# Kernel optimization log

Measured on AMD Instinct MI355X. Metric: run time of the kernel, lower is better.

The kernel has to match this reference:

```python
import jax, jax.numpy as jnp
import numpy as np

QMAX = 127.0
EPS = 1e-12


def _smooth_quant(x, col_scale):
    """Per-row int8 quantization of (x * col_scale).
    Returns (q, row_scale): q holds integer values in [-127, 127] (kept in f32,
    exactly representable), row_scale is abs-max/127 per row."""
    xs = x * col_scale                                  # [R, K]
    row_scale = jnp.max(jnp.abs(xs), axis=-1) / QMAX    # [R]
    row_scale = jnp.maximum(row_scale, EPS)
    q = jnp.clip(jnp.round(xs / row_scale[:, None]), -QMAX, QMAX)
    return q, row_scale


def setup_inputs() -> dict:
    key = jax.random.key(0)
    k1, k2, k3 = jax.random.split(key, 3)
    B, S, K, N = 4, 8192, 1024, 1024
    input_ = jax.random.normal(k1, (B, S, K), dtype=jnp.float32)
    weight = jax.random.normal(k2, (N, K), dtype=jnp.float32) * 0.02
    bias = jax.random.normal(k3, (N,), dtype=jnp.float32) * 0.01
    return {"input": input_, "weight": weight, "bias": bias}


def reference(input, weight, bias):
    x2 = input.reshape(-1, input.shape[-1])             # [M, K]
    # SmoothQuant smoothing scale: sqrt(colmax(|x|) * colmax(|w|)), shape [K]
    in_max = jnp.max(jnp.abs(x2), axis=0)
    w_max = jnp.max(jnp.abs(weight), axis=0)
    smooth_scale = jnp.sqrt(jnp.maximum(in_max * w_max, EPS))
    # quantize activations divided by smooth_scale, weights multiplied by it
    x_q, x_s = _smooth_quant(x2, 1.0 / smooth_scale)    # [M,K], [M]
    w_q, w_s = _smooth_quant(weight, smooth_scale)      # [N,K], [N]
    # int8 matmul (emulated exactly in f32) + row/col dequant scales + bias
    acc = x_q @ w_q.T                                   # [M, N]
    out = acc * x_s[:, None] * w_s[None, :] + bias
    return out.reshape(*input.shape[:-1], weight.shape[0])
```

## Files before the change

### kernel.cpp

```cpp
#include <hip/hip_runtime.h>


typedef int v4i __attribute__((ext_vector_type(4)));

__device__ __forceinline__ void gld_lds16(const void* g, void* l) {
    __builtin_amdgcn_global_load_lds(
        (const __attribute__((address_space(1))) void*)g,
        (__attribute__((address_space(3))) void*)l,
        16, 0, 0);
}

__device__ __forceinline__ void colmax_body(const float* __restrict__ src,
                                            int r0, int r1, int K,
                                            float* __restrict__ dst) {
    const int c = threadIdx.x * 4;
    float m0 = 0.f, m1 = 0.f, m2 = 0.f, m3 = 0.f;
    const float* p = src + (size_t)r0 * K + c;
#pragma unroll 8
    for (int r = r0; r < r1; ++r, p += K) {
        float4 v = *(const float4*)p;
        m0 = fmaxf(m0, fabsf(v.x));
        m1 = fmaxf(m1, fabsf(v.y));
        m2 = fmaxf(m2, fabsf(v.z));
        m3 = fmaxf(m3, fabsf(v.w));
    }
    float4 o; o.x = m0; o.y = m1; o.z = m2; o.w = m3;
    *(float4*)(dst + c) = o;
}

__global__ __launch_bounds__(256) void colmax_part_kernel(const float* __restrict__ src,
                                                          int rows, int rpb, int K,
                                                          float* __restrict__ partial) {
    int r0 = blockIdx.x * rpb;
    int r1 = r0 + rpb; if (r1 > rows) r1 = rows;
    colmax_body(src, r0, r1, K, partial + (size_t)blockIdx.x * K);
}

__global__ __launch_bounds__(256) void part2_fused_kernel(const float* __restrict__ p1x, int nx,
                                                          const float* __restrict__ w, int nw,
                                                          float* __restrict__ p2x,
                                                          float* __restrict__ pw, int K) {
    const int b = blockIdx.x;
    if (b < 16) {
        const int rpb = nx >> 4;
        colmax_body(p1x, b * rpb, (b + 1) * rpb, K, p2x + (size_t)b * K);
    } else {
        const int rpb = nw >> 4;
        colmax_body(w, (b - 16) * rpb, (b - 15) * rpb, K, pw + (size_t)(b - 16) * K);
    }
}

__global__ void finalize_kernel(const float* __restrict__ px, int nx,
                                const float* __restrict__ pw, int nw,
                                float* __restrict__ smooth, float* __restrict__ inv_s, int K) {
    int c = blockIdx.x * blockDim.x + threadIdx.x;
    if (c >= K) return;
    float mx = 0.f, mw = 0.f;
    for (int r = 0; r < nx; ++r) mx = fmaxf(mx, px[(size_t)r * K + c]);
    for (int r = 0; r < nw; ++r) mw = fmaxf(mw, pw[(size_t)r * K + c]);
    float s = sqrtf(fmaxf(mx * mw, 1e-12f));
    smooth[c] = s;
    inv_s[c]  = 1.0f / s;
}

__device__ __forceinline__ void quant_row_body(const float* __restrict__ src,
                                               const float* __restrict__ colscale,
                                               signed char* __restrict__ q,
                                               float* __restrict__ rowscale,
                                               int row, int K, int lane) {
    const float* srow = src + (size_t)row * K + lane * 16;
    const float* crow = colscale + lane * 16;
    float xs[16];
    float mv = 0.f;
#pragma unroll
    for (int i = 0; i < 4; ++i) {
        float4 v  = *(const float4*)(srow + i * 4);
        float4 cs = *(const float4*)(crow + i * 4);
        xs[i*4+0] = v.x * cs.x; xs[i*4+1] = v.y * cs.y;
        xs[i*4+2] = v.z * cs.z; xs[i*4+3] = v.w * cs.w;
        mv = fmaxf(mv, fmaxf(fmaxf(fabsf(xs[i*4+0]), fabsf(xs[i*4+1])),
                             fmaxf(fabsf(xs[i*4+2]), fabsf(xs[i*4+3]))));
    }
#pragma unroll
    for (int off = 32; off > 0; off >>= 1)
        mv = fmaxf(mv, __shfl_xor(mv, off, 64));
    const float rs = fmaxf(mv / 127.0f, 1e-12f);
    unsigned pk[4];
#pragma unroll
    for (int i = 0; i < 4; ++i) {
        float q0 = fminf(fmaxf(rintf(xs[i*4+0] / rs), -127.f), 127.f);
        float q1 = fminf(fmaxf(rintf(xs[i*4+1] / rs), -127.f), 127.f);
        float q2 = fminf(fmaxf(rintf(xs[i*4+2] / rs), -127.f), 127.f);
        float q3 = fminf(fmaxf(rintf(xs[i*4+3] / rs), -127.f), 127.f);
        int b0 = (int)q0, b1 = (int)q1, b2 = (int)q2, b3 = (int)q3;
        pk[i] = (unsigned)(b0 & 0xff) | ((unsigned)(b1 & 0xff) << 8)
              | ((unsigned)(b2 & 0xff) << 16) | ((unsigned)(b3 & 0xff) << 24);
    }
    *(uint4*)(q + (size_t)row * K + lane * 16) = make_uint4(pk[0], pk[1], pk[2], pk[3]);
    if (lane == 0) rowscale[row] = rs;
}

__global__ __launch_bounds__(256) void quant_fused_kernel(
    const float* __restrict__ w, const float* __restrict__ x,
    const float* __restrict__ smooth, const float* __restrict__ inv_s,
    signed char* __restrict__ w_q, float* __restrict__ w_s,
    signed char* __restrict__ x_q, float* __restrict__ x_s,
    int K, int wblocks) {
    const int wave = threadIdx.x >> 6, lane = threadIdx.x & 63;
    const int b = blockIdx.x;
    if (b < wblocks) {
        quant_row_body(w, smooth, w_q, w_s, b * 4 + wave, K, lane);
    } else {
        quant_row_body(x, inv_s, x_q, x_s, (b - wblocks) * 4 + wave, K, lane);
    }
}

__global__ __launch_bounds__(256, 2) void gemm_i8_kernel(
    const signed char* __restrict__ Aq,
    const signed char* __restrict__ Bq,
    const float* __restrict__ xs,
    const float* __restrict__ wsc,
    const float* __restrict__ bias,
    float* __restrict__ out,
    int M, int N, int K) {
    __shared__ __align__(16) signed char As[32768];
    __shared__ __align__(16) signed char Bs[32768];

    const int tid  = threadIdx.x;
    const int lane = tid & 63;
    const int wave = tid >> 6;
    const int wm = wave >> 1;
    const int wn = wave & 1;
    const int g  = lane >> 4;
    const int fr = lane & 15;

    const int NT = K >> 7;

    const int nwg = gridDim.x;
    const int wg  = (blockIdx.x & 7) * (nwg >> 3) + (blockIdx.x >> 3);
    const int nTn = N >> 7;
    const int tm = wg / nTn, tn = wg % nTn;
    const int bm = tm << 7, bn = tn << 7;

    const int srow = tid >> 2;
    const int schk = (tid & 3) ^ (srow & 3);
    const signed char* srcA0 = Aq + (size_t)(bm + srow) * K + schk * 16;
    const signed char* srcA1 = srcA0 + (size_t)64 * K;
    const signed char* srcB0 = Bq + (size_t)(bn + srow) * K + schk * 16;
    const signed char* srcB1 = srcB0 + (size_t)64 * K;
    const int ldsSt = tid * 16;

    const int swz   = (g ^ (fr & 3)) * 16;
    const int aBase = (wm * 64 + fr) * 64 + swz;
    const int bBase = (wn * 64 + fr) * 64 + swz;

    v4i acc[4][4] = {};
    v4i bf[4];

#define STAGE_A(T, KS) do { \
        const int go_ = (T) * 128 + (KS) * 64; \
        signed char* l_ = &As[((T) & 1) * 16384 + (KS) * 8192 + ldsSt]; \
        gld_lds16(srcA0 + go_, l_); \
        gld_lds16(srcA1 + go_, l_ + 4096); \
    } while (0)
#define STAGE_B(T, KS) do { \
        const int go_ = (T) * 128 + (KS) * 64; \
        signed char* l_ = &Bs[((T) & 1) * 16384 + (KS) * 8192 + ldsSt]; \
        gld_lds16(srcB0 + go_, l_); \
        gld_lds16(srcB1 + go_, l_ + 4096); \
    } while (0)

#define PHASE(BUF, KS, MH, STG, WAIT) \
    do { \
        const int hb_ = (BUF) * 16384 + (KS) * 8192; \
        v4i af[2]; \
        _Pragma("unroll") \
        for (int i = 0; i < 2; ++i) \
            af[i] = *(const v4i*)&As[hb_ + aBase + ((MH) * 2 + i) * 1024]; \
        if ((MH) == 0) { \
            _Pragma("unroll") \
            for (int j = 0; j < 4; ++j) \
                bf[j] = *(const v4i*)&Bs[hb_ + bBase + j * 1024]; \
        } \
        STG; \
        asm volatile("s_waitcnt " WAIT ::: "memory"); \
        asm volatile("s_barrier" ::: "memory"); \
        asm volatile("s_waitcnt lgkmcnt(0)" ::: "memory"); \
        __builtin_amdgcn_sched_barrier(0); \
        __builtin_amdgcn_s_setprio(1); \
        _Pragma("unroll") \
        for (int i = 0; i < 2; ++i) \
            _Pragma("unroll") \
            for (int j = 0; j < 4; ++j) \
                acc[(MH) * 2 + i][j] = __builtin_amdgcn_mfma_i32_16x16x64_i8( \
                    af[i], bf[j], acc[(MH) * 2 + i][j], 0, 0, 0); \
        __builtin_amdgcn_s_setprio(0); \
        asm volatile("s_barrier" ::: "memory"); \
    } while (0)

    STAGE_A(0, 0); STAGE_B(0, 0);
    STAGE_A(0, 1); STAGE_B(0, 1);
    STAGE_A(1, 0); STAGE_B(1, 0);
    asm volatile("s_waitcnt vmcnt(4)" ::: "memory");
    asm volatile("s_barrier" ::: "memory");

    for (int t = 0; t < NT - 2; ++t) {
        const int buf = t & 1;
        PHASE(buf, 0, 0, STAGE_A(t + 1, 1), "vmcnt(8)");
        PHASE(buf, 0, 1, STAGE_B(t + 1, 1), "vmcnt(8)");
        PHASE(buf, 1, 0, STAGE_A(t + 2, 0), "vmcnt(8)");
        PHASE(buf, 1, 1, STAGE_B(t + 2, 0), "vmcnt(8)");
    }
    {
        const int t = NT - 2, buf = t & 1;
        PHASE(buf, 0, 0, STAGE_A(t + 1, 1), "vmcnt(8)");
        PHASE(buf, 0, 1, STAGE_B(t + 1, 1), "vmcnt(8)");
        PHASE(buf, 1, 0, (void)0, "vmcnt(8)");
        PHASE(buf, 1, 1, (void)0, "vmcnt(4)");
    }
    {
        const int buf = (NT - 1) & 1;
        PHASE(buf, 0, 0, (void)0, "vmcnt(4)");
        PHASE(buf, 0, 1, (void)0, "vmcnt(0)");
        PHASE(buf, 1, 0, (void)0, "vmcnt(0)");
        PHASE(buf, 1, 1, (void)0, "vmcnt(0)");
    }
#undef PHASE
#undef STAGE_A
#undef STAGE_B

    const int orow0 = bm + wm * 64 + g * 4;
    const int ocol0 = bn + wn * 64 + fr;
    float wv[4], bvv[4];
#pragma unroll
    for (int j = 0; j < 4; ++j) {
        wv[j]  = wsc[ocol0 + j * 16];
        bvv[j] = bias[ocol0 + j * 16];
    }
#pragma unroll
    for (int i = 0; i < 4; ++i) {
#pragma unroll
        for (int r = 0; r < 4; ++r) {
            const int row = orow0 + i * 16 + r;
            const float xv = xs[row];
            float* op = out + (size_t)row * N + ocol0;
#pragma unroll
            for (int j = 0; j < 4; ++j)
                op[j * 16] = (float)acc[i][j][r] * xv * wv[j] + bvv[j];
        }
    }
}

extern "C" void kernel_launch(void* const* d_in, const int* in_sizes, int n_in,
                              void* d_out, int out_size, void* d_ws, size_t ws_size,
                              hipStream_t stream) {
    const float* x    = (const float*)d_in[0];
    const float* w    = (const float*)d_in[1];
    const float* bias = (const float*)d_in[2];
    float* out = (float*)d_out;

    const int N = in_sizes[2];
    const int K = in_sizes[1] / N;
    const int M = in_sizes[0] / K;

    char* ws = (char*)d_ws;
    float* p1x       = (float*)(ws);
    float* p2x       = (float*)(ws + 2097152);
    float* pw        = (float*)(ws + 2162688);
    float* smooth    = (float*)(ws + 2228224);
    float* inv_s     = (float*)(ws + 2232320);
    float* w_s       = (float*)(ws + 2236416);
    float* x_s       = (float*)(ws + 2240512);
    signed char* x_q = (signed char*)(ws + 2371584);
    signed char* w_q = x_q + (size_t)M * K;

    colmax_part_kernel<<<512, 256, 0, stream>>>(x, M, 64, K, p1x);
    part2_fused_kernel<<<32, 256, 0, stream>>>(p1x, 512, w, N, p2x, pw, K);
    finalize_kernel<<<(K + 255) / 256, 256, 0, stream>>>(p2x, 16, pw, 16, smooth, inv_s, K);
    quant_fused_kernel<<<N / 4 + M / 4, 256, 0, stream>>>(w, x, smooth, inv_s,
                                                          w_q, w_s, x_q, x_s, K, N / 4);
    gemm_i8_kernel<<<(M / 128) * (N / 128), 256, 0, stream>>>(x_q, w_q, x_s, w_s, bias, out, M, N, K);
}
```

Measured before the change: 321.3 us.

## Use 8-wave 512-thread GEMM workgroups with 64x32 per-wave tiles and merged staging

```diff
diff --git a/kernel.cpp b/kernel.cpp
--- a/kernel.cpp
+++ b/kernel.cpp
@@ -115,7 +115,7 @@
     }
 }
 
-__global__ __launch_bounds__(256, 2) void gemm_i8_kernel(
+__global__ __launch_bounds__(512, 4) void gemm_i8_kernel(
     const signed char* __restrict__ Aq,
     const signed char* __restrict__ Bq,
     const float* __restrict__ xs,
@@ -129,8 +129,8 @@
     const int tid  = threadIdx.x;
     const int lane = tid & 63;
     const int wave = tid >> 6;
-    const int wm = wave >> 1;
-    const int wn = wave & 1;
+    const int wm = wave >> 2;
+    const int wn = wave & 3;
     const int g  = lane >> 4;
     const int fr = lane & 15;
 
@@ -143,97 +143,94 @@
     const int bm = tm << 7, bn = tn << 7;
 
     const int srow = tid >> 2;
-    const int schk = (tid & 3) ^ (srow & 3);
+    const int schk = (tid & 3) ^ ((tid >> 3) & 3);
     const signed char* srcA0 = Aq + (size_t)(bm + srow) * K + schk * 16;
-    const signed char* srcA1 = srcA0 + (size_t)64 * K;
     const signed char* srcB0 = Bq + (size_t)(bn + srow) * K + schk * 16;
-    const signed char* srcB1 = srcB0 + (size_t)64 * K;
     const int ldsSt = tid * 16;
 
-    const int swz   = (g ^ (fr & 3)) * 16;
+    const int swz   = (g ^ ((fr >> 1) & 3)) * 16;
     const int aBase = (wm * 64 + fr) * 64 + swz;
-    const int bBase = (wn * 64 + fr) * 64 + swz;
-
-    v4i acc[4][4] = {};
-    v4i bf[4];
-
-#define STAGE_A(T, KS) do { \
+    const int bBase = (wn * 32 + fr) * 64 + swz;
+
+    v4i acc[4][2] = {};
+
+#define STAGE_AB(T, KS) do { \
         const int go_ = (T) * 128 + (KS) * 64; \
-        signed char* l_ = &As[((T) & 1) * 16384 + (KS) * 8192 + ldsSt]; \
-        gld_lds16(srcA0 + go_, l_); \
-        gld_lds16(srcA1 + go_, l_ + 4096); \
+        const int lo_ = ((T) & 1) * 16384 + (KS) * 8192 + ldsSt; \
+        gld_lds16(srcA0 + go_, &As[lo_]); \
+        gld_lds16(srcB0 + go_, &Bs[lo_]); \
     } while (0)
-#define STAGE_B(T, KS) do { \
-        const int go_ = (T) * 128 + (KS) * 64; \
-        signed char* l_ = &Bs[((T) & 1) * 16384 + (KS) * 8192 + ldsSt]; \
-        gld_lds16(srcB0 + go_, l_); \
-        gld_lds16(srcB1 + go_, l_ + 4096); \
-    } while (0)
-
-#define PHASE(BUF, KS, MH, STG, WAIT) \
-    do { \
+
+#define PH_READS(BUF, KS) \
         const int hb_ = (BUF) * 16384 + (KS) * 8192; \
-        v4i af[2]; \
+        v4i af[4], bf[2]; \
         _Pragma("unroll") \
-        for (int i = 0; i < 2; ++i) \
-            af[i] = *(const v4i*)&As[hb_ + aBase + ((MH) * 2 + i) * 1024]; \
-        if ((MH) == 0) { \
-            _Pragma("unroll") \
-            for (int j = 0; j < 4; ++j) \
-                bf[j] = *(const v4i*)&Bs[hb_ + bBase + j * 1024]; \
-        } \
-        STG; \
-        asm volatile("s_waitcnt " WAIT ::: "memory"); \
-        asm volatile("s_barrier" ::: "memory"); \
+        for (int i = 0; i < 4; ++i) \
+            af[i] = *(const v4i*)&As[hb_ + aBase + i * 1024]; \
+        _Pragma("unroll") \
+        for (int j = 0; j < 2; ++j) \
+            bf[j] = *(const v4i*)&Bs[hb_ + bBase + j * 1024];
+
+#define PH_MFMA() \
         asm volatile("s_waitcnt lgkmcnt(0)" ::: "memory"); \
         __builtin_amdgcn_sched_barrier(0); \
         __builtin_amdgcn_s_setprio(1); \
         _Pragma("unroll") \
-        for (int i = 0; i < 2; ++i) \
+        for (int i = 0; i < 4; ++i) \
             _Pragma("unroll") \
-            for (int j = 0; j < 4; ++j) \
-                acc[(MH) * 2 + i][j] = __builtin_amdgcn_mfma_i32_16x16x64_i8( \
-                    af[i], bf[j], acc[(MH) * 2 + i][j], 0, 0, 0); \
+            for (int j = 0; j < 2; ++j) \
+                acc[i][j] = __builtin_amdgcn_mfma_i32_16x16x64_i8( \
+                    af[i], bf[j], acc[i][j], 0, 0, 0); \
         __builtin_amdgcn_s_setprio(0); \
+        asm volatile("s_barrier" ::: "memory");
+
+#define PHASE_W(BUF, KS, STG, WAIT) \
+    do { \
+        PH_READS(BUF, KS) \
+        STG; \
+        asm volatile("s_waitcnt " WAIT ::: "memory"); \
         asm volatile("s_barrier" ::: "memory"); \
+        PH_MFMA() \
     } while (0)
 
-    STAGE_A(0, 0); STAGE_B(0, 0);
-    STAGE_A(0, 1); STAGE_B(0, 1);
-    STAGE_A(1, 0); STAGE_B(1, 0);
+#define PHASE_NW(BUF, KS) \
+    do { \
+        PH_READS(BUF, KS) \
+        PH_MFMA() \
+    } while (0)
+
+    STAGE_AB(0, 0);
+    STAGE_AB(0, 1);
+    STAGE_AB(1, 0);
     asm volatile("s_waitcnt vmcnt(4)" ::: "memory");
     asm volatile("s_barrier" ::: "memory");
 
     for (int t = 0; t < NT - 2; ++t) {
         const int buf = t & 1;
-        PHASE(buf, 0, 0, STAGE_A(t + 1, 1), "vmcnt(8)");
-        PHASE(buf, 0, 1, STAGE_B(t + 1, 1), "vmcnt(8)");
-        PHASE(buf, 1, 0, STAGE_A(t + 2, 0), "vmcnt(8)");
-        PHASE(buf, 1, 1, STAGE_B(t + 2, 0), "vmcnt(8)");
+        PHASE_W(buf, 0, STAGE_AB(t + 1, 1), "vmcnt(4)");
+        PHASE_W(buf, 1, STAGE_AB(t + 2, 0), "vmcnt(4)");
     }
     {
         const int t = NT - 2, buf = t & 1;
-        PHASE(buf, 0, 0, STAGE_A(t + 1, 1), "vmcnt(8)");
-        PHASE(buf, 0, 1, STAGE_B(t + 1, 1), "vmcnt(8)");
-        PHASE(buf, 1, 0, (void)0, "vmcnt(8)");
-        PHASE(buf, 1, 1, (void)0, "vmcnt(4)");
+        PHASE_W(buf, 0, STAGE_AB(t + 1, 1), "vmcnt(4)");
+        PHASE_W(buf, 1, (void)0, "vmcnt(2)");
     }
     {
         const int buf = (NT - 1) & 1;
-        PHASE(buf, 0, 0, (void)0, "vmcnt(4)");
-        PHASE(buf, 0, 1, (void)0, "vmcnt(0)");
-        PHASE(buf, 1, 0, (void)0, "vmcnt(0)");
-        PHASE(buf, 1, 1, (void)0, "vmcnt(0)");
-    }
-#undef PHASE
-#undef STAGE_A
-#undef STAGE_B
+        PHASE_W(buf, 0, (void)0, "vmcnt(0)");
+        PHASE_NW(buf, 1);
+    }
+#undef PHASE_W
+#undef PHASE_NW
+#undef PH_READS
+#undef PH_MFMA
+#undef STAGE_AB
 
     const int orow0 = bm + wm * 64 + g * 4;
-    const int ocol0 = bn + wn * 64 + fr;
-    float wv[4], bvv[4];
-#pragma unroll
-    for (int j = 0; j < 4; ++j) {
+    const int ocol0 = bn + wn * 32 + fr;
+    float wv[2], bvv[2];
+#pragma unroll
+    for (int j = 0; j < 2; ++j) {
         wv[j]  = wsc[ocol0 + j * 16];
         bvv[j] = bias[ocol0 + j * 16];
     }
@@ -245,7 +242,7 @@
             const float xv = xs[row];
             float* op = out + (size_t)row * N + ocol0;
 #pragma unroll
-            for (int j = 0; j < 4; ++j)
+            for (int j = 0; j < 2; ++j)
                 op[j * 16] = (float)acc[i][j][r] * xv * wv[j] + bvv[j];
         }
     }
@@ -279,5 +276,5 @@
     finalize_kernel<<<(K + 255) / 256, 256, 0, stream>>>(p2x, 16, pw, 16, smooth, inv_s, K);
     quant_fused_kernel<<<N / 4 + M / 4, 256, 0, stream>>>(w, x, smooth, inv_s,
                                                           w_q, w_s, x_q, x_s, K, N / 4);
-    gemm_i8_kernel<<<(M / 128) * (N / 128), 256, 0, stream>>>(x_q, w_q, x_s, w_s, bias, out, M, N, K);
-}
+    gemm_i8_kernel<<<(M / 128) * (N / 128), 512, 0, stream>>>(x_q, w_q, x_s, w_s, bias, out, M, N, K);
+}
```

New measurement: 312.8 us. 1.03x faster.
